# Kernel optimization log

Measured on AMD Instinct MI355X. Metric: run time of the kernel, lower is better.

Reference implementation:

```python
import jax, jax.numpy as jnp
import numpy as np

N_EXPERTS = 8
TOP_K = 2


def setup_inputs() -> dict:
    key = jax.random.key(0)
    ks = jax.random.split(key, 5)
    B, T, C, H, E = 4, 2048, 1024, 2048, N_EXPERTS
    scale = 0.02
    return {
        "x": jax.random.normal(ks[0], (B, T, C), dtype=jnp.float32),
        "w_gate": jax.random.normal(ks[1], (C, E), dtype=jnp.float32) * scale,
        "wi": jax.random.normal(ks[2], (E, C, H), dtype=jnp.float32) * scale,
        "wg": jax.random.normal(ks[3], (E, C, H), dtype=jnp.float32) * scale,
        "wo": jax.random.normal(ks[4], (E, H, C), dtype=jnp.float32) * scale,
    }


def reference(x, w_gate, wi, wg, wo):
    # x: [B,T,C]; w_gate: [C,E]; wi/wg: [E,C,H]; wo: [E,H,C]
    B, T, C = x.shape
    E = w_gate.shape[-1]
    logits = jnp.einsum("btc,ce->bte", x, w_gate)
    gates = jax.nn.softmax(logits, axis=-1)                 # [B,T,E]
    topk_vals, topk_idx = jax.lax.top_k(gates, TOP_K)       # [B,T,k]
    # combine weights: sum over slots of gate value where expert selected
    onehot = jax.nn.one_hot(topk_idx, E, dtype=x.dtype)     # [B,T,k,E]
    combine = jnp.einsum("btk,btke->bte", topk_vals, onehot)  # [B,T,E]

    x_flat = x.reshape(B * T, C)
    combine_flat = combine.reshape(B * T, E)
    out = jnp.zeros_like(x_flat)
    # small fixed loop over experts (structurally distinct weight slices)
    for e in range(E):
        up = x_flat @ wi[e]                                  # [N,H]
        gate = x_flat @ wg[e]                                # [N,H]
        y = (jax.nn.silu(gate) * up) @ wo[e]                 # [N,C]
        out = out + combine_flat[:, e:e + 1] * y
    return out.reshape(B, T, C)
```

## Files before the change

kernel.cpp:

```cpp
#include <hip/hip_runtime.h>
#include <hip/hip_bf16.h>


#define N_TOK 8192
#define C_DIM 1024
#define H_DIM 2048
#define E_NUM 8

typedef __attribute__((ext_vector_type(8))) short short8;
typedef __attribute__((ext_vector_type(4))) float f32x4;

__device__ __forceinline__ unsigned short f2bf(float f) {
    unsigned int u = __float_as_uint(f);
    unsigned int r = (u + 0x7FFFu + ((u >> 16) & 1u)) >> 16;
    return (unsigned short)r;
}

__device__ __forceinline__ f32x4 mfma16(short8 a, short8 b, f32x4 c) {
    return __builtin_amdgcn_mfma_f32_16x16x32_bf16(a, b, c, 0, 0, 0);
}

__global__ __launch_bounds__(256) void k_gate(
    const float* __restrict__ x, const float* __restrict__ wgate,
    int* __restrict__ counts, int* __restrict__ tlist,
    float* __restrict__ combine, unsigned short* __restrict__ xbf)
{
    int wid = threadIdx.x >> 6;
    int lane = threadIdx.x & 63;
    int token = blockIdx.x * 4 + wid;
    const float* xr = x + (size_t)token * C_DIM;
    unsigned short* xbr = xbf + (size_t)token * C_DIM;

    float p[E_NUM] = {0.f,0.f,0.f,0.f,0.f,0.f,0.f,0.f};
    #pragma unroll
    for (int i = 0; i < C_DIM / 64; ++i) {
        int c = i * 64 + lane;
        float xv = xr[c];
        xbr[c] = f2bf(xv);
        const float4* wr = reinterpret_cast<const float4*>(wgate + (size_t)c * E_NUM);
        float4 w0 = wr[0], w1 = wr[1];
        p[0] += xv * w0.x; p[1] += xv * w0.y; p[2] += xv * w0.z; p[3] += xv * w0.w;
        p[4] += xv * w1.x; p[5] += xv * w1.y; p[6] += xv * w1.z; p[7] += xv * w1.w;
    }
    #pragma unroll
    for (int e = 0; e < E_NUM; ++e) {
        #pragma unroll
        for (int s = 32; s > 0; s >>= 1) p[e] += __shfl_xor(p[e], s, 64);
    }
    if (lane == 0) {
        float m = p[0];
        #pragma unroll
        for (int e = 1; e < E_NUM; ++e) m = fmaxf(m, p[e]);
        float g[E_NUM]; float den = 0.f;
        #pragma unroll
        for (int e = 0; e < E_NUM; ++e) { g[e] = expf(p[e] - m); den += g[e]; }
        float inv = 1.f / den;
        #pragma unroll
        for (int e = 0; e < E_NUM; ++e) g[e] *= inv;
        int i1 = 0;
        #pragma unroll
        for (int e = 1; e < E_NUM; ++e) if (g[e] > g[i1]) i1 = e;
        int i2 = (i1 == 0) ? 1 : 0;
        #pragma unroll
        for (int e = 0; e < E_NUM; ++e) if (e != i1 && g[e] > g[i2]) i2 = e;
        #pragma unroll
        for (int e = 0; e < E_NUM; ++e)
            combine[(size_t)token * E_NUM + e] = (e == i1 || e == i2) ? g[e] : 0.f;
        int p1 = atomicAdd(&counts[i1], 1);
        tlist[i1 * N_TOK + p1] = token;
        int p2 = atomicAdd(&counts[i2], 1);
        tlist[i2 * N_TOK + p2] = token;
    }
}

__global__ __launch_bounds__(256) void k_upgate(
    const unsigned short* __restrict__ xbf,
    const float* __restrict__ Wi, const float* __restrict__ Wg,
    const int* __restrict__ counts, const int* __restrict__ tlist,
    unsigned short* __restrict__ hbuf)
{
    __shared__ unsigned short smem[10240];
    int e = blockIdx.z;
    int cnt = counts[e];
    int mbase = blockIdx.y * 128;
    if (mbase >= cnt) return;
    int n0 = blockIdx.x * 64;
    int off = 0;
    for (int i = 0; i < e; ++i) off += counts[i];

    int t = threadIdx.x;
    int wid = t >> 6, lane = t & 63;
    int fl = lane & 15, kg = lane >> 4;
    int wm = (wid >> 1) * 64, wn = (wid & 1) * 32;

    int ar = t >> 1, ahalf = t & 1;
    int agrow = mbase + ar;
    int tok = (agrow < cnt) ? tlist[e * N_TOK + agrow] : 0;
    const unsigned short* asrc = xbf + (size_t)tok * C_DIM;

    int mat = wid >> 1, khalf = wid & 1;
    const float* W = (mat ? Wg : Wi) + (size_t)e * C_DIM * H_DIM;

    unsigned short* sA = smem;
    unsigned short* sB = smem + 5120;

    f32x4 accu[4][2], accg[4][2];
    #pragma unroll
    for (int fm = 0; fm < 4; ++fm)
        #pragma unroll
        for (int fn = 0; fn < 2; ++fn) {
            accu[fm][fn] = (f32x4){0.f,0.f,0.f,0.f};
            accg[fm][fn] = (f32x4){0.f,0.f,0.f,0.f};
        }

    for (int k0 = 0; k0 < C_DIM; k0 += 32) {
        {
            const uint4* s = reinterpret_cast<const uint4*>(asrc + k0 + ahalf * 16);
            uint4 v0 = s[0], v1 = s[1];
            uint4* d = reinterpret_cast<uint4*>(sA + ar * 40 + ahalf * 16);
            d[0] = v0; d[1] = v1;
        }
        {
            union { unsigned short u[16]; uint4 v[2]; } col;
            const float* wp = W + (size_t)(k0 + khalf * 16) * H_DIM + n0 + lane;
            #pragma unroll
            for (int i = 0; i < 16; ++i) col.u[i] = f2bf(wp[(size_t)i * H_DIM]);
            uint4* d = reinterpret_cast<uint4*>(sB + mat * 2560 + lane * 40 + khalf * 16);
            d[0] = col.v[0]; d[1] = col.v[1];
        }
        __syncthreads();
        short8 a[4];
        #pragma unroll
        for (int fm = 0; fm < 4; ++fm)
            a[fm] = *reinterpret_cast<const short8*>(sA + (wm + fm * 16 + fl) * 40 + kg * 8);
        short8 bi[2], bg[2];
        #pragma unroll
        for (int fn = 0; fn < 2; ++fn) {
            bi[fn] = *reinterpret_cast<const short8*>(sB + (wn + fn * 16 + fl) * 40 + kg * 8);
            bg[fn] = *reinterpret_cast<const short8*>(sB + 2560 + (wn + fn * 16 + fl) * 40 + kg * 8);
        }
        #pragma unroll
        for (int fm = 0; fm < 4; ++fm)
            #pragma unroll
            for (int fn = 0; fn < 2; ++fn) {
                accu[fm][fn] = mfma16(a[fm], bi[fn], accu[fm][fn]);
                accg[fm][fn] = mfma16(a[fm], bg[fn], accg[fm][fn]);
            }
        __syncthreads();
    }

    unsigned short* sh = smem;
    #pragma unroll
    for (int fm = 0; fm < 4; ++fm)
        #pragma unroll
        for (int fn = 0; fn < 2; ++fn)
            #pragma unroll
            for (int j = 0; j < 4; ++j) {
                float uv = accu[fm][fn][j];
                float gv = accg[fm][fn][j];
                float hv = (gv / (1.f + expf(-gv))) * uv;
                int row = wm + fm * 16 + kg * 4 + j;
                int coln = wn + fn * 16 + fl;
                sh[row * 72 + coln] = f2bf(hv);
            }
    __syncthreads();
    if (agrow < cnt) {
        const uint4* s = reinterpret_cast<const uint4*>(sh + ar * 72 + ahalf * 32);
        uint4* d = reinterpret_cast<uint4*>(hbuf + (size_t)(off + agrow) * H_DIM + n0 + ahalf * 32);
        d[0] = s[0]; d[1] = s[1]; d[2] = s[2]; d[3] = s[3];
    }
}

__global__ __launch_bounds__(256) void k_down(
    const unsigned short* __restrict__ hbuf, const float* __restrict__ Wo,
    const int* __restrict__ counts, const int* __restrict__ tlist,
    const float* __restrict__ combine, float* __restrict__ out)
{
    __shared__ unsigned short smem[7680];
    __shared__ int stok[128];
    __shared__ float scw[128];
    int e = blockIdx.z;
    int cnt = counts[e];
    int mbase = blockIdx.y * 128;
    if (mbase >= cnt) return;
    int n0 = blockIdx.x * 64;
    int off = 0;
    for (int i = 0; i < e; ++i) off += counts[i];

    int t = threadIdx.x;
    int wid = t >> 6, lane = t & 63;
    int fl = lane & 15, kg = lane >> 4;
    int wm = (wid >> 1) * 64, wn = (wid & 1) * 32;

    if (t < 128) {
        int grow = mbase + t;
        int v = grow < cnt;
        int tk = v ? tlist[e * N_TOK + grow] : 0;
        stok[t] = tk;
        scw[t] = v ? combine[(size_t)tk * E_NUM + e] : 0.f;
    }

    int ar = t >> 1, ahalf = t & 1;
    int hr = off + mbase + ar; if (hr > N_TOK * 2 - 1) hr = N_TOK * 2 - 1;
    const unsigned short* asrc = hbuf + (size_t)hr * H_DIM;
    const float* W = Wo + (size_t)e * H_DIM * C_DIM;

    unsigned short* sA = smem;
    unsigned short* sB = smem + 5120;

    f32x4 acc[4][2];
    #pragma unroll
    for (int fm = 0; fm < 4; ++fm)
        #pragma unroll
        for (int fn = 0; fn < 2; ++fn) acc[fm][fn] = (f32x4){0.f,0.f,0.f,0.f};

    for (int k0 = 0; k0 < H_DIM; k0 += 32) {
        {
            const uint4* s = reinterpret_cast<const uint4*>(asrc + k0 + ahalf * 16);
            uint4 v0 = s[0], v1 = s[1];
            uint4* d = reinterpret_cast<uint4*>(sA + ar * 40 + ahalf * 16);
            d[0] = v0; d[1] = v1;
        }
        {
            union { unsigned short u[8]; uint4 v; } col;
            const float* wp = W + (size_t)(k0 + wid * 8) * C_DIM + n0 + lane;
            #pragma unroll
            for (int i = 0; i < 8; ++i) col.u[i] = f2bf(wp[(size_t)i * C_DIM]);
            *reinterpret_cast<uint4*>(sB + lane * 40 + wid * 8) = col.v;
        }
        __syncthreads();
        short8 a[4], b[2];
        #pragma unroll
        for (int fm = 0; fm < 4; ++fm)
            a[fm] = *reinterpret_cast<const short8*>(sA + (wm + fm * 16 + fl) * 40 + kg * 8);
        #pragma unroll
        for (int fn = 0; fn < 2; ++fn)
            b[fn] = *reinterpret_cast<const short8*>(sB + (wn + fn * 16 + fl) * 40 + kg * 8);
        #pragma unroll
        for (int fm = 0; fm < 4; ++fm)
            #pragma unroll
            for (int fn = 0; fn < 2; ++fn)
                acc[fm][fn] = mfma16(a[fm], b[fn], acc[fm][fn]);
        __syncthreads();
    }

    #pragma unroll
    for (int fm = 0; fm < 4; ++fm)
        #pragma unroll
        for (int fn = 0; fn < 2; ++fn)
            #pragma unroll
            for (int j = 0; j < 4; ++j) {
                int rl = wm + fm * 16 + kg * 4 + j;
                if (mbase + rl < cnt) {
                    float v = acc[fm][fn][j] * scw[rl];
                    atomicAdd(out + (size_t)stok[rl] * C_DIM + n0 + wn + fn * 16 + fl, v);
                }
            }
}

extern "C" void kernel_launch(void* const* d_in, const int* in_sizes, int n_in,
                              void* d_out, int out_size, void* d_ws, size_t ws_size,
                              hipStream_t stream)
{
    const float* x     = (const float*)d_in[0];
    const float* wgate = (const float*)d_in[1];
    const float* wi    = (const float*)d_in[2];
    const float* wg    = (const float*)d_in[3];
    const float* wo    = (const float*)d_in[4];
    float* out = (float*)d_out;
    char* ws = (char*)d_ws;

    int* counts      = (int*)(ws + 0);
    int* tlist       = (int*)(ws + 1024);
    float* combine   = (float*)(ws + 263168);
    unsigned short* xbf = (unsigned short*)(ws + 1048576);
    unsigned short* h   = (unsigned short*)(ws + 17825792);

    hipMemsetAsync(counts, 0, 64, stream);
    hipMemsetAsync(d_out, 0, (size_t)out_size * sizeof(float), stream);

    k_gate<<<dim3(N_TOK / 4), dim3(256), 0, stream>>>(x, wgate, counts, tlist, combine, xbf);
    k_upgate<<<dim3(H_DIM / 64, N_TOK / 128, E_NUM), dim3(256), 0, stream>>>(
        xbf, wi, wg, counts, tlist, h);
    k_down<<<dim3(C_DIM / 64, N_TOK / 128, E_NUM), dim3(256), 0, stream>>>(
        h, wo, counts, tlist, combine, out);
}
```

Measured before the change: 847.4 us.

## Pre-convert expert weights to swizzled bf16 tiles and use direct global-to-LDS loads

Adds a kernel that converts the fp32 expert weights into bf16, pre-transposed, swizzled 64x64 tiles in workspace. The up/gate and down GEMMs then stage A and B operands with global_load_lds 16-byte direct copies instead of converting fp32 weights inside every block. This aims to remove repeated per-block fp32-to-bf16 conversion and halve weight read traffic during the GEMMs. In exchange it adds a conversion pass over all weights on every call and needs roughly 190MB of workspace, keeping the old path as a fallback.

```diff
diff --git a/kernel.cpp b/kernel.cpp
--- a/kernel.cpp
+++ b/kernel.cpp
@@ -9,6 +9,7 @@
 
 typedef __attribute__((ext_vector_type(8))) short short8;
 typedef __attribute__((ext_vector_type(4))) float f32x4;
+typedef unsigned int u32;
 
 __device__ __forceinline__ unsigned short f2bf(float f) {
     unsigned int u = __float_as_uint(f);
@@ -18,6 +19,12 @@
 
 __device__ __forceinline__ f32x4 mfma16(short8 a, short8 b, f32x4 c) {
     return __builtin_amdgcn_mfma_f32_16x16x32_bf16(a, b, c, 0, 0, 0);
+}
+
+__device__ __forceinline__ void gl_lds16(const void* g, void* l) {
+    __builtin_amdgcn_global_load_lds(
+        (const __attribute__((address_space(1))) u32*)g,
+        (__attribute__((address_space(3))) u32*)l, 16, 0, 0);
 }
 
 __global__ __launch_bounds__(256) void k_gate(
@@ -73,7 +80,244 @@
     }
 }
 
-__global__ __launch_bounds__(256) void k_upgate(
+__global__ __launch_bounds__(256) void k_wconv(
+    const float* __restrict__ wi, const float* __restrict__ wg, const float* __restrict__ wo,
+    unsigned short* __restrict__ wit, unsigned short* __restrict__ wgt, unsigned short* __restrict__ wot)
+{
+    __shared__ unsigned short sT[64 * 80];
+    int m = blockIdx.z;
+    int e = blockIdx.y;
+    const float* src; unsigned short* dst; int N; int ktb;
+    if (m == 0)      { src = wi; dst = wit; N = H_DIM; ktb = 4; }
+    else if (m == 1) { src = wg; dst = wgt; N = H_DIM; ktb = 4; }
+    else             { src = wo; dst = wot; N = C_DIM; ktb = 5; }
+    int K = (m == 2) ? H_DIM : C_DIM;
+    int tile = blockIdx.x;
+    int nt = tile >> ktb;
+    int kt = tile & ((1 << ktb) - 1);
+    src += (size_t)e * K * N + (size_t)(kt * 64) * N + nt * 64;
+    dst += ((size_t)e * 512 + tile) * 4096;
+
+    int t = threadIdx.x;
+    int kl = t >> 2, nq = (t & 3) << 4;
+    const float4* s4 = reinterpret_cast<const float4*>(src + (size_t)kl * N + nq);
+    #pragma unroll
+    for (int q = 0; q < 4; ++q) {
+        float4 v = s4[q];
+        sT[(nq + q * 4 + 0) * 80 + kl] = f2bf(v.x);
+        sT[(nq + q * 4 + 1) * 80 + kl] = f2bf(v.y);
+        sT[(nq + q * 4 + 2) * 80 + kl] = f2bf(v.z);
+        sT[(nq + q * 4 + 3) * 80 + kl] = f2bf(v.w);
+    }
+    __syncthreads();
+    #pragma unroll
+    for (int q = 0; q < 2; ++q) {
+        int ci = t * 2 + q;
+        int nl = ci >> 3;
+        int kc = (ci & 7) ^ (nl & 7);
+        uint4 v = *reinterpret_cast<const uint4*>(sT + nl * 80 + kc * 8);
+        *reinterpret_cast<uint4*>((char*)dst + ci * 16) = v;
+    }
+}
+
+__global__ __launch_bounds__(256) void k_upgate_f(
+    const unsigned short* __restrict__ xbf,
+    const unsigned short* __restrict__ wit, const unsigned short* __restrict__ wgt,
+    const int* __restrict__ counts, const int* __restrict__ tlist,
+    unsigned short* __restrict__ hbuf)
+{
+    __shared__ unsigned short smem[16384];
+    int e = blockIdx.z;
+    int cnt = counts[e];
+    int mbase = blockIdx.y * 128;
+    if (mbase >= cnt) return;
+    int nt = blockIdx.x;
+    int off = 0;
+    for (int i = 0; i < e; ++i) off += counts[i];
+
+    int t = threadIdx.x, w = t >> 6, lane = t & 63;
+    int fl = lane & 15, kg = lane >> 4;
+    int wm = (w >> 1) * 64, wn = (w & 1) * 32;
+
+    int rsub = lane >> 3;
+    int cb = lane & 7;
+    int swz = (cb ^ rsub) << 4;
+    const char* aptr[4];
+    #pragma unroll
+    for (int j = 0; j < 4; ++j) {
+        int r = w * 32 + j * 8 + rsub;
+        int tok = (mbase + r < cnt) ? tlist[e * N_TOK + mbase + r] : 0;
+        aptr[j] = (const char*)(xbf + (size_t)tok * C_DIM) + swz;
+    }
+    int mat = w >> 1, bc = w & 1;
+    const unsigned short* wtb = mat ? wgt : wit;
+    const char* bptr = (const char*)wtb + ((size_t)e * 512 + (size_t)nt * 16) * 8192
+                       + bc * 4096 + lane * 16;
+
+    f32x4 accu[4][2], accg[4][2];
+    #pragma unroll
+    for (int fm = 0; fm < 4; ++fm)
+        #pragma unroll
+        for (int fn = 0; fn < 2; ++fn) {
+            accu[fm][fn] = (f32x4){0.f,0.f,0.f,0.f};
+            accg[fm][fn] = (f32x4){0.f,0.f,0.f,0.f};
+        }
+
+    for (int kt = 0; kt < 16; ++kt) {
+        #pragma unroll
+        for (int j = 0; j < 4; ++j)
+            gl_lds16(aptr[j] + (kt << 7), smem + w * 2048 + j * 512);
+        #pragma unroll
+        for (int j = 0; j < 4; ++j)
+            gl_lds16(bptr + (size_t)kt * 8192 + j * 1024,
+                     smem + 8192 + mat * 4096 + bc * 2048 + j * 512);
+        __syncthreads();
+        #pragma unroll
+        for (int kk = 0; kk < 2; ++kk) {
+            short8 a[4], bu[2], bg[2];
+            #pragma unroll
+            for (int fm = 0; fm < 4; ++fm) {
+                int r = wm + fm * 16 + fl;
+                int xo = ((kk * 64 + kg * 16) ^ ((r & 7) << 4)) >> 1;
+                a[fm] = *reinterpret_cast<const short8*>(smem + r * 64 + xo);
+            }
+            #pragma unroll
+            for (int fn = 0; fn < 2; ++fn) {
+                int n = wn + fn * 16 + fl;
+                int xo = ((kk * 64 + kg * 16) ^ ((n & 7) << 4)) >> 1;
+                bu[fn] = *reinterpret_cast<const short8*>(smem + 8192 + n * 64 + xo);
+                bg[fn] = *reinterpret_cast<const short8*>(smem + 12288 + n * 64 + xo);
+            }
+            #pragma unroll
+            for (int fm = 0; fm < 4; ++fm)
+                #pragma unroll
+                for (int fn = 0; fn < 2; ++fn) {
+                    accu[fm][fn] = mfma16(a[fm], bu[fn], accu[fm][fn]);
+                    accg[fm][fn] = mfma16(a[fm], bg[fn], accg[fm][fn]);
+                }
+        }
+        __syncthreads();
+    }
+
+    unsigned short* sh = smem;
+    #pragma unroll
+    for (int fm = 0; fm < 4; ++fm)
+        #pragma unroll
+        for (int fn = 0; fn < 2; ++fn)
+            #pragma unroll
+            for (int j = 0; j < 4; ++j) {
+                float uv = accu[fm][fn][j];
+                float gv = accg[fm][fn][j];
+                float hv = (gv / (1.f + expf(-gv))) * uv;
+                int row = wm + fm * 16 + kg * 4 + j;
+                int coln = wn + fn * 16 + fl;
+                sh[row * 80 + coln] = f2bf(hv);
+            }
+    __syncthreads();
+    int ar = t >> 1, ahalf = t & 1;
+    if (mbase + ar < cnt) {
+        const uint4* s = reinterpret_cast<const uint4*>(sh + ar * 80 + ahalf * 32);
+        uint4* d = reinterpret_cast<uint4*>(hbuf + (size_t)(off + mbase + ar) * H_DIM + nt * 64 + ahalf * 32);
+        d[0] = s[0]; d[1] = s[1]; d[2] = s[2]; d[3] = s[3];
+    }
+}
+
+__global__ __launch_bounds__(256) void k_down_f(
+    const unsigned short* __restrict__ hbuf, const unsigned short* __restrict__ wot,
+    const int* __restrict__ counts, const int* __restrict__ tlist,
+    const float* __restrict__ combine, float* __restrict__ out)
+{
+    __shared__ unsigned short smem[12288];
+    __shared__ int stok[128];
+    __shared__ float scw[128];
+    int e = blockIdx.z;
+    int cnt = counts[e];
+    int mbase = blockIdx.y * 128;
+    if (mbase >= cnt) return;
+    int nt = blockIdx.x;
+    int off = 0;
+    for (int i = 0; i < e; ++i) off += counts[i];
+
+    int t = threadIdx.x, w = t >> 6, lane = t & 63;
+    int fl = lane & 15, kg = lane >> 4;
+    int wm = (w >> 1) * 64, wn = (w & 1) * 32;
+
+    if (t < 128) {
+        int grow = mbase + t;
+        int v = grow < cnt;
+        int tk = v ? tlist[e * N_TOK + grow] : 0;
+        stok[t] = tk;
+        scw[t] = v ? combine[(size_t)tk * E_NUM + e] : 0.f;
+    }
+
+    int rsub = lane >> 3;
+    int cb = lane & 7;
+    int swz = (cb ^ rsub) << 4;
+    const char* aptr[4];
+    #pragma unroll
+    for (int j = 0; j < 4; ++j) {
+        int r = w * 32 + j * 8 + rsub;
+        int hr = off + mbase + r;
+        if (hr > N_TOK * 2 - 1) hr = N_TOK * 2 - 1;
+        aptr[j] = (const char*)(hbuf + (size_t)hr * H_DIM) + swz;
+    }
+    const char* bptr = (const char*)wot + ((size_t)e * 512 + (size_t)nt * 32) * 8192
+                       + w * 2048 + lane * 16;
+
+    f32x4 acc[4][2];
+    #pragma unroll
+    for (int fm = 0; fm < 4; ++fm)
+        #pragma unroll
+        for (int fn = 0; fn < 2; ++fn) acc[fm][fn] = (f32x4){0.f,0.f,0.f,0.f};
+
+    for (int kt = 0; kt < 32; ++kt) {
+        #pragma unroll
+        for (int j = 0; j < 4; ++j)
+            gl_lds16(aptr[j] + (kt << 7), smem + w * 2048 + j * 512);
+        #pragma unroll
+        for (int j = 0; j < 2; ++j)
+            gl_lds16(bptr + (size_t)kt * 8192 + j * 1024,
+                     smem + 8192 + w * 1024 + j * 512);
+        __syncthreads();
+        #pragma unroll
+        for (int kk = 0; kk < 2; ++kk) {
+            short8 a[4], b[2];
+            #pragma unroll
+            for (int fm = 0; fm < 4; ++fm) {
+                int r = wm + fm * 16 + fl;
+                int xo = ((kk * 64 + kg * 16) ^ ((r & 7) << 4)) >> 1;
+                a[fm] = *reinterpret_cast<const short8*>(smem + r * 64 + xo);
+            }
+            #pragma unroll
+            for (int fn = 0; fn < 2; ++fn) {
+                int n = wn + fn * 16 + fl;
+                int xo = ((kk * 64 + kg * 16) ^ ((n & 7) << 4)) >> 1;
+                b[fn] = *reinterpret_cast<const short8*>(smem + 8192 + n * 64 + xo);
+            }
+            #pragma unroll
+            for (int fm = 0; fm < 4; ++fm)
+                #pragma unroll
+                for (int fn = 0; fn < 2; ++fn)
+                    acc[fm][fn] = mfma16(a[fm], b[fn], acc[fm][fn]);
+        }
+        __syncthreads();
+    }
+
+    #pragma unroll
+    for (int fm = 0; fm < 4; ++fm)
+        #pragma unroll
+        for (int fn = 0; fn < 2; ++fn)
+            #pragma unroll
+            for (int j = 0; j < 4; ++j) {
+                int rl = wm + fm * 16 + kg * 4 + j;
+                if (mbase + rl < cnt) {
+                    float v = acc[fm][fn][j] * scw[rl];
+                    atomicAdd(out + (size_t)stok[rl] * C_DIM + nt * 64 + wn + fn * 16 + fl, v);
+                }
+            }
+}
+
+__global__ __launch_bounds__(256) void k_upgate_s(
     const unsigned short* __restrict__ xbf,
     const float* __restrict__ Wi, const float* __restrict__ Wg,
     const int* __restrict__ counts, const int* __restrict__ tlist,
@@ -171,7 +415,7 @@
     }
 }
 
-__global__ __launch_bounds__(256) void k_down(
+__global__ __launch_bounds__(256) void k_down_s(
     const unsigned short* __restrict__ hbuf, const float* __restrict__ Wo,
     const int* __restrict__ counts, const int* __restrict__ tlist,
     const float* __restrict__ combine, float* __restrict__ out)
@@ -276,12 +520,26 @@
     unsigned short* xbf = (unsigned short*)(ws + 1048576);
     unsigned short* h   = (unsigned short*)(ws + 17825792);
 
+    const size_t NEED = 190840832ull;
+
     hipMemsetAsync(counts, 0, 64, stream);
     hipMemsetAsync(d_out, 0, (size_t)out_size * sizeof(float), stream);
 
-    k_gate<<<dim3(N_TOK / 4), dim3(256), 0, stream>>>(x, wgate, counts, tlist, combine, xbf);
-    k_upgate<<<dim3(H_DIM / 64, N_TOK / 128, E_NUM), dim3(256), 0, stream>>>(
-        xbf, wi, wg, counts, tlist, h);
-    k_down<<<dim3(C_DIM / 64, N_TOK / 128, E_NUM), dim3(256), 0, stream>>>(
-        h, wo, counts, tlist, combine, out);
-}
+    if (ws_size >= NEED) {
+        unsigned short* wit = (unsigned short*)(ws + 90177536ull);
+        unsigned short* wgt = (unsigned short*)(ws + 123731968ull);
+        unsigned short* wot = (unsigned short*)(ws + 157286400ull);
+        k_wconv<<<dim3(512, 8, 3), dim3(256), 0, stream>>>(wi, wg, wo, wit, wgt, wot);
+        k_gate<<<dim3(N_TOK / 4), dim3(256), 0, stream>>>(x, wgate, counts, tlist, combine, xbf);
+        k_upgate_f<<<dim3(32, N_TOK / 128, E_NUM), dim3(256), 0, stream>>>(
+            xbf, wit, wgt, counts, tlist, h);
+        k_down_f<<<dim3(16, N_TOK / 128, E_NUM), dim3(256), 0, stream>>>(
+            h, wot, counts, tlist, combine, out);
+    } else {
+        k_gate<<<dim3(N_TOK / 4), dim3(256), 0, stream>>>(x, wgate, counts, tlist, combine, xbf);
+        k_upgate_s<<<dim3(H_DIM / 64, N_TOK / 128, E_NUM), dim3(256), 0, stream>>>(
+            xbf, wi, wg, counts, tlist, h);
+        k_down_s<<<dim3(C_DIM / 64, N_TOK / 128, E_NUM), dim3(256), 0, stream>>>(
+            h, wo, counts, tlist, combine, out);
+    }
+}
```

Result: faster. 766.0 us (-9.6%).
